# Kernel optimization log

Hardware: AMD Instinct MI355X
Metric: run time of the kernel (lower is better)

The kernel has to match this reference:

```python
import jax, jax.numpy as jnp
import numpy as np

B, N, F = 8, 1024, 256
OUT, REL = 256, 16
NADJ = 7  # ((2 relations + consecutive) * 2 for backward) + self link


def setup_inputs() -> dict:
    key = jax.random.key(0)
    k0, k1, k2, k3, k4 = jax.random.split(key, 5)
    features = jax.random.normal(k0, (B, N, F), dtype=jnp.float32)
    A1 = jax.random.uniform(k1, (B, N, N), dtype=jnp.float32)
    A2 = jax.random.uniform(k2, (B, N, N), dtype=jnp.float32)
    # learned params: one (F+REL, OUT) weight per adjacency matrix, edge embeddings init 'ones', bias (N, OUT)
    W = jax.random.normal(k3, (NADJ, F + REL, OUT), dtype=jnp.float32) * 0.05
    W_edges = jnp.ones((NADJ, REL), dtype=jnp.float32)
    b = jax.random.uniform(k4, (N, OUT), dtype=jnp.float32, minval=-0.05, maxval=0.05)
    return {"features": features, "A1": A1, "A2": A2, "W": W, "W_edges": W_edges, "b": b}


def reference(features, A1, A2, W, W_edges, b):
    # eye = A[0] * zeros(N) + eye(N)  -> batch-broadcast identity [B,N,N]
    eye = jnp.zeros_like(A1) + jnp.eye(N, dtype=A1.dtype)
    # original rolls along axis 0 (batch) of the broadcast identity (faithful replication)
    shifted = jnp.roll(eye, 1, axis=0)
    A_fwd = [A1, A2, shifted]                      # relations + consecutive link
    A_list = A_fwd + [jnp.swapaxes(a, 1, 2) for a in A_fwd]  # backward links
    A_list.append(eye)                             # self links
    A = jnp.stack(A_list, axis=0)                  # [R,B,N,N]

    # concat(features, tile(W_edges[r])) @ W[r] == features @ W[r][:F] + W_edges[r] @ W[r][F:]
    HW = jnp.einsum('bnf,rfo->rbno', features, W[:, :F]) \
         + jnp.einsum('rd,rdo->ro', W_edges, W[:, F:])[:, None, None, :]  # [R,B,N,OUT]
    AHW = jnp.einsum('rbnm,rbmo->rbno', A, HW)     # batched adjacency matmul
    out = jnp.max(AHW, axis=0) + b                 # max-aggregate over relations, add bias
    return out                                     # activation = linear
```

## Files before the change

### kernel.cpp

```cpp
#include <hip/hip_runtime.h>
#include <hip/hip_bf16.h>

#define B_ 8
#define N_ 1024
#define F_ 256
#define OUT_ 256
#define REL_ 16
#define NADJ_ 7

typedef __attribute__((ext_vector_type(8))) _Float16 f16x8;
typedef __attribute__((ext_vector_type(4))) _Float16 f16x4;
typedef __attribute__((ext_vector_type(4))) float f32x4;

__device__ __forceinline__ void gll16(const _Float16* g, _Float16* l) {
    __builtin_amdgcn_global_load_lds(
        (const __attribute__((address_space(1))) void*)g,
        (__attribute__((address_space(3))) void*)l, 16, 0, 0);
}

__device__ __forceinline__ f16x8 cvt8(float4 a, float4 b) {
    return f16x8{(_Float16)a.x, (_Float16)a.y, (_Float16)a.z, (_Float16)a.w,
                 (_Float16)b.x, (_Float16)b.y, (_Float16)b.z, (_Float16)b.w};
}

#define MEMPIN() asm volatile("" ::: "memory")

__constant__ const int c_perm[7] = {0, 1, 3, 4, 2, 5, 6};

__global__ __launch_bounds__(256) void prep_kernel(const float* __restrict__ W,
                                                   const float* __restrict__ We,
                                                   const float* __restrict__ feat,
                                                   float* __restrict__ cb,
                                                   _Float16* __restrict__ WTp,
                                                   _Float16* __restrict__ Fe) {
    int bid = blockIdx.x, tid = threadIdx.x;
    if (bid < 7) {
        int idx = bid * 256 + tid;
        int j = idx / OUT_, o = idx % OUT_;
        int r = c_perm[j];
        const float* Wr = W + (size_t)r * (F_ + REL_) * OUT_;
        float s = 0.f;
#pragma unroll
        for (int d = 0; d < REL_; ++d) s += We[r * REL_ + d] * Wr[(F_ + d) * OUT_ + o];
        cb[idx] = s;
    } else if (bid < 1799) {
        int idx = (bid - 7) * 256 + tid;
        int j = idx >> 16, rem = idx & 65535, o = rem >> 8, f = rem & 255;
        int r = c_perm[j];
        WTp[idx] = (_Float16)W[((size_t)r * (F_ + REL_) + f) * OUT_ + o];
    } else {
        int i = (bid - 1799) * 256 + tid;
        size_t base = (size_t)i * 8;
        float4 a = *(const float4*)(feat + base);
        float4 b = *(const float4*)(feat + base + 4);
        *(f16x8*)(Fe + base) = cvt8(a, b);
    }
}

__global__ __launch_bounds__(256) void hw7_kernel(const _Float16* __restrict__ Fe,
                                                  const _Float16* __restrict__ WTp,
                                                  const float* __restrict__ cb,
                                                  _Float16* __restrict__ HWT,
                                                  _Float16* __restrict__ HWN) {
    __shared__ _Float16 S[3 * 8192];
    const int bid = blockIdx.x, tid = threadIdx.x;
    const int z = bid / 128, rem = bid % 128, bx = rem & 63, by = rem >> 6;
    const bool tr = (z < 4);
    const _Float16* A  = tr ? (WTp + (size_t)z * 65536) : Fe;
    const _Float16* Bt = tr ? Fe : (WTp + (size_t)z * 65536);
    const int m0 = (tr ? by : bx) * 128;
    const int n0 = (tr ? bx : by) * 128;
    const int wave = tid >> 6, lane = tid & 63, lm = lane & 15, q = lane >> 4;
    const int wr = (wave >> 1) * 64, wc = (wave & 1) * 64;
    const int srow = tid >> 2, sk = (tid & 3) * 8;
    const _Float16* ga0 = A + (size_t)(m0 + srow) * F_ + sk;
    const _Float16* ga1 = ga0 + (size_t)64 * F_;
    const _Float16* gb0 = Bt + (size_t)(n0 + srow) * F_ + sk;
    const _Float16* gb1 = gb0 + (size_t)64 * F_;

    f32x4 acc[4][4] = {};
    const int NT = 8;

    {
        gll16(ga0, S + tid * 8);
        gll16(ga1, S + 2048 + tid * 8);
        gll16(gb0, S + 4096 + tid * 8);
        gll16(gb1, S + 6144 + tid * 8);
        MEMPIN();
        gll16(ga0 + 32, S + 8192 + tid * 8);
        gll16(ga1 + 32, S + 8192 + 2048 + tid * 8);
        gll16(gb0 + 32, S + 8192 + 4096 + tid * 8);
        gll16(gb1 + 32, S + 8192 + 6144 + tid * 8);
        asm volatile("s_waitcnt vmcnt(4)" ::: "memory");
        __builtin_amdgcn_s_barrier();
    }
    int cs = 0, ns = 1, fs = 2;
    for (int t = 0; t < NT; ++t) {
        if (t + 2 < NT) {
            const int k = (t + 2) * 32;
            _Float16* sb = S + fs * 8192;
            gll16(ga0 + k, sb + tid * 8);
            gll16(ga1 + k, sb + 2048 + tid * 8);
            gll16(gb0 + k, sb + 4096 + tid * 8);
            gll16(gb1 + k, sb + 6144 + tid * 8);
        }
        {
            const _Float16* Au = S + cs * 8192;
            const _Float16* Bu = Au + 4096;
            f16x8 af[4], bf[4];
#pragma unroll
            for (int i = 0; i < 4; ++i) af[i] = *(const f16x8*)(Au + (wr + i * 16 + lm) * 32 + q * 8);
#pragma unroll
            for (int j = 0; j < 4; ++j) bf[j] = *(const f16x8*)(Bu + (wc + j * 16 + lm) * 32 + q * 8);
            __builtin_amdgcn_s_setprio(1);
#pragma unroll
            for (int i = 0; i < 4; ++i)
#pragma unroll
                for (int j = 0; j < 4; ++j)
                    acc[i][j] = __builtin_amdgcn_mfma_f32_16x16x32_f16(af[i], bf[j], acc[i][j], 0, 0, 0);
            __builtin_amdgcn_s_setprio(0);
        }
        if (t + 1 < NT) {
            if (t + 2 < NT) asm volatile("s_waitcnt vmcnt(4)" ::: "memory");
            else            asm volatile("s_waitcnt vmcnt(0)" ::: "memory");
            __builtin_amdgcn_s_barrier();
        }
        int tmp = cs; cs = ns; ns = fs; fs = tmp;
    }
    const float* cbz = cb + (size_t)z * 256;
    if (tr) {
        _Float16* C = HWT + (size_t)z * ((size_t)256 * 8192);
#pragma unroll
        for (int i = 0; i < 4; ++i)
#pragma unroll
            for (int j = 0; j < 4; ++j)
#pragma unroll
                for (int g = 0; g < 4; ++g) {
                    int row = wr + i * 16 + q * 4 + g;
                    int col = wc + j * 16 + lm;
                    float v = acc[i][j][g] + cbz[m0 + row];
                    C[(size_t)(m0 + row) * 8192 + (n0 + col)] = (_Float16)v;
                }
    } else {
        _Float16* C = HWN + (size_t)(z - 4) * ((size_t)8192 * 256);
#pragma unroll
        for (int i = 0; i < 4; ++i)
#pragma unroll
            for (int j = 0; j < 4; ++j)
#pragma unroll
                for (int g = 0; g < 4; ++g) {
                    int row = wr + i * 16 + q * 4 + g;
                    int col = wc + j * 16 + lm;
                    float v = acc[i][j][g] + cbz[n0 + col];
                    C[(size_t)(m0 + row) * 256 + (n0 + col)] = (_Float16)v;
                }
    }
}

__global__ __launch_bounds__(256) void p2_kernel(const float* __restrict__ A1,
                                                 const float* __restrict__ A2,
                                                 const _Float16* __restrict__ HWT,
                                                 _Float16* __restrict__ AHW) {
    __shared__ _Float16 As[3 * 4096];
    __shared__ _Float16 Bs[3 * 4096];
    const int d = blockIdx.x;
    const int xcd = d & 7, slot = d >> 3;
    const int zz = xcd + 8 * (slot >> 4);
    const int member = (slot >> 3) & 1;
    const int mt = slot & 7;
    const int rr = zz >> 3, b = zz & 7;

    const size_t slab = (size_t)B_ * N_ * OUT_;
    const _Float16* Bt = HWT + (size_t)rr * (256 * 8192) + (size_t)b * 1024;
    _Float16* C = AHW + (size_t)rr * slab + (size_t)b * (N_ * OUT_);
    const int m0 = mt * 128, n0 = member * 128;
    const int tid = threadIdx.x;
    const int wave = tid >> 6, lane = tid & 63, lm = lane & 15, q = lane >> 4;
    const int wr = (wave >> 1) * 64, wc = (wave & 1) * 64;
    const int srow = tid >> 2, sk = (tid & 3) * 8;
    const _Float16* gb0 = Bt + (size_t)(n0 + srow) * 8192 + sk;
    const _Float16* gb1 = gb0 + (size_t)64 * 8192;

    const float* Ag = ((rr & 1) ? A2 : A1) + (size_t)b * N_ * N_;
    f32x4 acc[4][4] = {};
    const int NT = 32;

    auto mfma_step = [&](int st) {
        const _Float16* Au = As + st * 4096;
        const _Float16* Bu = Bs + st * 4096;
        f16x8 af[4], bf[4];
#pragma unroll
        for (int i = 0; i < 4; ++i)
            af[i] = *(const f16x8*)(Au + (wr + i * 16 + lm) * 32 + ((q ^ i) * 8));
#pragma unroll
        for (int j = 0; j < 4; ++j)
            bf[j] = *(const f16x8*)(Bu + (wc + j * 16 + lm) * 32 + q * 8);
        __builtin_amdgcn_s_setprio(1);
#pragma unroll
        for (int i = 0; i < 4; ++i)
#pragma unroll
            for (int j = 0; j < 4; ++j)
                acc[i][j] = __builtin_amdgcn_mfma_f32_16x16x32_f16(af[i], bf[j], acc[i][j], 0, 0, 0);
        __builtin_amdgcn_s_setprio(0);
    };

    if (rr < 2) {
        const float* Ag0 = Ag + (size_t)(m0 + srow) * N_ + sk;
        const float* Ag1 = Ag0 + (size_t)64 * N_;
        const int sx = ((tid & 3) ^ ((tid >> 6) & 3)) * 8;
        float4 p0, p1, p2, p3;
        {
            float4 q0 = *(const float4*)(Ag0);
            float4 q1 = *(const float4*)(Ag0 + 4);
            float4 q2 = *(const float4*)(Ag1);
            float4 q3 = *(const float4*)(Ag1 + 4);
            *(f16x8*)(As + srow * 32 + sx) = cvt8(q0, q1);
            *(f16x8*)(As + 2048 + srow * 32 + sx) = cvt8(q2, q3);
            MEMPIN();
            gll16(gb0, Bs + tid * 8);
            gll16(gb1, Bs + 2048 + tid * 8);
            MEMPIN();
            p0 = *(const float4*)(Ag0 + 32);
            p1 = *(const float4*)(Ag0 + 36);
            p2 = *(const float4*)(Ag1 + 32);
            p3 = *(const float4*)(Ag1 + 36);
            MEMPIN();
            gll16(gb0 + 32, Bs + 4096 + tid * 8);
            gll16(gb1 + 32, Bs + 4096 + 2048 + tid * 8);
            asm volatile("s_waitcnt vmcnt(6)" ::: "memory");
            asm volatile("s_waitcnt lgkmcnt(0)" ::: "memory");
            __builtin_amdgcn_s_barrier();
        }
        int cs = 0, ns = 1, fs = 2;
        for (int t = 0; t < NT; ++t) {
            if (t + 1 < NT) {
                _Float16* la = As + ns * 4096 + srow * 32 + sx;
                *(f16x8*)(la) = cvt8(p0, p1);
                *(f16x8*)(la + 2048) = cvt8(p2, p3);
            }
            MEMPIN();
            if (t + 2 < NT) {
                const int k2 = (t + 2) * 32;
                p0 = *(const float4*)(Ag0 + k2);
                p1 = *(const float4*)(Ag0 + k2 + 4);
                p2 = *(const float4*)(Ag1 + k2);
                p3 = *(const float4*)(Ag1 + k2 + 4);
                MEMPIN();
                gll16(gb0 + k2, Bs + fs * 4096 + tid * 8);
                gll16(gb1 + k2, Bs + fs * 4096 + 2048 + tid * 8);
            }
            mfma_step(cs);
            if (t + 1 < NT) {
                if (t + 2 < NT) asm volatile("s_waitcnt vmcnt(6)" ::: "memory");
                else            asm volatile("s_waitcnt vmcnt(0)" ::: "memory");
                asm volatile("s_waitcnt lgkmcnt(0)" ::: "memory");
                __builtin_amdgcn_s_barrier();
            }
            int tmp = cs; cs = ns; ns = fs; fs = tmp;
        }
    } else {
        const int kk4 = (tid >> 5) * 4;
        const int ms4 = (tid & 31) * 4;
        const int tsw = ((ms4 >> 4) & 3) << 3;
        const int wof = ms4 * 32 + (kk4 ^ tsw);
        const float* gA0 = Ag + (size_t)kk4 * N_ + m0 + ms4;
        float4 r0, r1, r2, r3;
        {
            float4 q0 = *(const float4*)(gA0);
            float4 q1 = *(const float4*)(gA0 + N_);
            float4 q2 = *(const float4*)(gA0 + 2 * N_);
            float4 q3 = *(const float4*)(gA0 + 3 * N_);
            _Float16* wp = As + wof;
            *(f16x4*)(wp + 0 * 32) = f16x4{(_Float16)q0.x, (_Float16)q1.x, (_Float16)q2.x, (_Float16)q3.x};
            *(f16x4*)(wp + 1 * 32) = f16x4{(_Float16)q0.y, (_Float16)q1.y, (_Float16)q2.y, (_Float16)q3.y};
            *(f16x4*)(wp + 2 * 32) = f16x4{(_Float16)q0.z, (_Float16)q1.z, (_Float16)q2.z, (_Float16)q3.z};
            *(f16x4*)(wp + 3 * 32) = f16x4{(_Float16)q0.w, (_Float16)q1.w, (_Float16)q2.w, (_Float16)q3.w};
            MEMPIN();
            gll16(gb0, Bs + tid * 8);
            gll16(gb1, Bs + 2048 + tid * 8);
            MEMPIN();
            const float* p = gA0 + (size_t)32 * N_;
            r0 = *(const float4*)(p);
            r1 = *(const float4*)(p + N_);
            r2 = *(const float4*)(p + 2 * N_);
            r3 = *(const float4*)(p + 3 * N_);
            MEMPIN();
            gll16(gb0 + 32, Bs + 4096 + tid * 8);
            gll16(gb1 + 32, Bs + 4096 + 2048 + tid * 8);
            asm volatile("s_waitcnt vmcnt(6)" ::: "memory");
            asm volatile("s_waitcnt lgkmcnt(0)" ::: "memory");
            __builtin_amdgcn_s_barrier();
        }
        const float* gp = gA0 + (size_t)64 * N_;
        int cs = 0, ns = 1, fs = 2;
        for (int t = 0; t < NT; ++t) {
            if (t + 1 < NT) {
                _Float16* wp = As + ns * 4096 + wof;
                *(f16x4*)(wp + 0 * 32) = f16x4{(_Float16)r0.x, (_Float16)r1.x, (_Float16)r2.x, (_Float16)r3.x};
                *(f16x4*)(wp + 1 * 32) = f16x4{(_Float16)r0.y, (_Float16)r1.y, (_Float16)r2.y, (_Float16)r3.y};
                *(f16x4*)(wp + 2 * 32) = f16x4{(_Float16)r0.z, (_Float16)r1.z, (_Float16)r2.z, (_Float16)r3.z};
                *(f16x4*)(wp + 3 * 32) = f16x4{(_Float16)r0.w, (_Float16)r1.w, (_Float16)r2.w, (_Float16)r3.w};
            }
            MEMPIN();
            if (t + 2 < NT) {
                r0 = *(const float4*)(gp);
                r1 = *(const float4*)(gp + N_);
                r2 = *(const float4*)(gp + 2 * N_);
                r3 = *(const float4*)(gp + 3 * N_);
                gp += (size_t)32 * N_;
                MEMPIN();
                const int k2 = (t + 2) * 32;
                gll16(gb0 + k2, Bs + fs * 4096 + tid * 8);
                gll16(gb1 + k2, Bs + fs * 4096 + 2048 + tid * 8);
            }
            mfma_step(cs);
            if (t + 1 < NT) {
                if (t + 2 < NT) asm volatile("s_waitcnt vmcnt(6)" ::: "memory");
                else            asm volatile("s_waitcnt vmcnt(0)" ::: "memory");
                asm volatile("s_waitcnt lgkmcnt(0)" ::: "memory");
                __builtin_amdgcn_s_barrier();
            }
            int tmp = cs; cs = ns; ns = fs; fs = tmp;
        }
    }
#pragma unroll
    for (int i = 0; i < 4; ++i)
#pragma unroll
        for (int j = 0; j < 4; ++j)
#pragma unroll
            for (int g = 0; g < 4; ++g) {
                int row = wr + i * 16 + q * 4 + g;
                int col = wc + j * 16 + lm;
                C[(size_t)(m0 + row) * 256 + (n0 + col)] = (_Float16)acc[i][j][g];
            }
}

__global__ __launch_bounds__(256) void max_kernel(const _Float16* __restrict__ AHW,
                                                  const _Float16* __restrict__ HWN,
                                                  const float* __restrict__ bias,
                                                  float* __restrict__ out) {
    size_t i = ((size_t)blockIdx.x * 256 + threadIdx.x) * 8;
    const size_t slab = (size_t)B_ * N_ * OUT_;
    float m[8];
    f16x8 v = *(const f16x8*)(AHW + i);
#pragma unroll
    for (int e = 0; e < 8; ++e) m[e] = (float)v[e];
#pragma unroll
    for (int rr = 1; rr < 4; ++rr) {
        f16x8 w = *(const f16x8*)(AHW + rr * slab + i);
#pragma unroll
        for (int e = 0; e < 8; ++e) m[e] = fmaxf(m[e], (float)w[e]);
    }
#pragma unroll
    for (int j = 0; j < 3; ++j) {
        f16x8 w = *(const f16x8*)(HWN + j * slab + i);
#pragma unroll
        for (int e = 0; e < 8; ++e) m[e] = fmaxf(m[e], (float)w[e]);
    }
    size_t bidx = i & ((size_t)N_ * OUT_ - 1);
    float4 b0 = *(const float4*)(bias + bidx);
    float4 b1 = *(const float4*)(bias + bidx + 4);
    float4 o0 = {m[0] + b0.x, m[1] + b0.y, m[2] + b0.z, m[3] + b0.w};
    float4 o1 = {m[4] + b1.x, m[5] + b1.y, m[6] + b1.z, m[7] + b1.w};
    *(float4*)(out + i) = o0;
    *(float4*)(out + i + 4) = o1;
}

__global__ void cbias_kernel(const float* __restrict__ W, const float* __restrict__ We,
                             float* __restrict__ c) {
    int idx = blockIdx.x * 256 + threadIdx.x;
    if (idx >= NADJ_ * OUT_) return;
    int r = idx / OUT_, o = idx % OUT_;
    const float* Wr = W + (size_t)r * (F_ + REL_) * OUT_;
    float s = 0.f;
#pragma unroll
    for (int d = 0; d < REL_; ++d) s += We[r * REL_ + d] * Wr[(F_ + d) * OUT_ + o];
    c[idx] = s;
}

__global__ __launch_bounds__(256) void hw_kernel(const float* __restrict__ feat,
                                                 const float* __restrict__ W,
                                                 const float* __restrict__ cb,
                                                 _Float16* __restrict__ HWb) {
    __shared__ _Float16 As[64][32];
    __shared__ _Float16 Bs[64][32];
    const int mt = blockIdx.x, ct = blockIdx.y;
    const int tid = threadIdx.x, wave = tid >> 6, lane = tid & 63;
    const int r = (ct * 64) / OUT_;
    const int o0 = (ct * 64) % OUT_;
    const float* Bg = W + (size_t)r * (F_ + REL_) * OUT_ + o0;
    const int m0 = mt * 64;
    const int lm = lane & 15, q = lane >> 4;
    f32x4 acc[4] = {};
    for (int k0 = 0; k0 < F_; k0 += 32) {
        {
            int seg = (tid & 3) * 8, m = tid >> 2;
            const float* src = feat + (size_t)(m0 + m) * F_ + k0 + seg;
#pragma unroll
            for (int j = 0; j < 8; ++j) As[m][seg + j] = (_Float16)src[j];
        }
        {
            int kk = tid >> 3, ns = (tid & 7) * 8;
            const float* src = Bg + (size_t)(k0 + kk) * OUT_ + ns;
#pragma unroll
            for (int j = 0; j < 8; ++j) Bs[ns + j][kk] = (_Float16)src[j];
        }
        __syncthreads();
        f16x8 a = *(const f16x8*)&As[wave * 16 + lm][q * 8];
#pragma unroll
        for (int c4 = 0; c4 < 4; ++c4) {
            f16x8 b = *(const f16x8*)&Bs[c4 * 16 + lm][q * 8];
            acc[c4] = __builtin_amdgcn_mfma_f32_16x16x32_f16(a, b, acc[c4], 0, 0, 0);
        }
        __syncthreads();
    }
#pragma unroll
    for (int c4 = 0; c4 < 4; ++c4)
#pragma unroll
        for (int g = 0; g < 4; ++g) {
            int row = wave * 16 + (lane >> 4) * 4 + g;
            int col = c4 * 16 + lm;
            float v = acc[c4][g] + cb[r * OUT_ + o0 + col];
            HWb[((size_t)r * B_ * N_ + m0 + row) * OUT_ + o0 + col] = (_Float16)v;
        }
}

__global__ __launch_bounds__(256) void agg_kernel(const float* __restrict__ A1,
                                                  const float* __restrict__ A2,
                                                  const _Float16* __restrict__ HWb,
                                                  const float* __restrict__ bias,
                                                  float* __restrict__ out) {
    __shared__ _Float16 As[64][32];
    __shared__ _Float16 Bs[64][32];
    const int b = blockIdx.z, nt = blockIdx.y, ot = blockIdx.x;
    const int tid = threadIdx.x, wave = tid >> 6, lane = tid & 63;
    const int n0 = nt * 64, o0 = ot * 64;
    const int lm = lane & 15, q = lane >> 4;
    const size_t rstride = (size_t)B_ * N_ * OUT_;
    f32x4 mx[4];
#pragma unroll
    for (int i = 0; i < 4; ++i) mx[i] = f32x4{-1e30f, -1e30f, -1e30f, -1e30f};
#pragma unroll 1
    for (int rr = 0; rr < 4; ++rr) {
        const float* Ag = ((rr & 1) ? A2 : A1) + (size_t)b * N_ * N_;
        const bool tr = (rr >= 2);
        const int r = (rr < 2) ? rr : rr + 1;
        const _Float16* Bg = HWb + (size_t)r * rstride + (size_t)b * N_ * OUT_ + o0;
        f32x4 acc[4] = {};
        for (int k0 = 0; k0 < N_; k0 += 32) {
            if (!tr) {
                int seg = (tid & 3) * 8, m = tid >> 2;
                const float* src = Ag + (size_t)(n0 + m) * N_ + k0 + seg;
#pragma unroll
                for (int j = 0; j < 8; ++j) As[m][seg + j] = (_Float16)src[j];
            } else {
                int kk = tid >> 3, ms = (tid & 7) * 8;
                const float* src = Ag + (size_t)(k0 + kk) * N_ + n0 + ms;
#pragma unroll
                for (int j = 0; j < 8; ++j) As[ms + j][kk] = (_Float16)src[j];
            }
            {
                int kk = tid >> 3, ns = (tid & 7) * 8;
                const _Float16* src = Bg + (size_t)(k0 + kk) * OUT_ + ns;
#pragma unroll
                for (int j = 0; j < 8; ++j) Bs[ns + j][kk] = src[j];
            }
            __syncthreads();
            f16x8 a = *(const f16x8*)&As[wave * 16 + lm][q * 8];
#pragma unroll
            for (int c4 = 0; c4 < 4; ++c4) {
                f16x8 bb = *(const f16x8*)&Bs[c4 * 16 + lm][q * 8];
                acc[c4] = __builtin_amdgcn_mfma_f32_16x16x32_f16(a, bb, acc[c4], 0, 0, 0);
            }
            __syncthreads();
        }
#pragma unroll
        for (int c4 = 0; c4 < 4; ++c4)
#pragma unroll
            for (int g = 0; g < 4; ++g) mx[c4][g] = fmaxf(mx[c4][g], acc[c4][g]);
    }
#pragma unroll
    for (int c4 = 0; c4 < 4; ++c4)
#pragma unroll
        for (int g = 0; g < 4; ++g) {
            int row = wave * 16 + (lane >> 4) * 4 + g;
            int col = c4 * 16 + lm;
            size_t pos = ((size_t)b * N_ + n0 + row) * OUT_ + o0 + col;
            float v = mx[c4][g];
            v = fmaxf(v, (float)HWb[2 * rstride + pos]);
            v = fmaxf(v, (float)HWb[5 * rstride + pos]);
            v = fmaxf(v, (float)HWb[6 * rstride + pos]);
            out[pos] = v + bias[((size_t)(n0 + row)) * OUT_ + o0 + col];
        }
}

extern "C" void kernel_launch(void* const* d_in, const int* in_sizes, int n_in,
                              void* d_out, int out_size, void* d_ws, size_t ws_size,
                              hipStream_t stream) {
    const float* feat = (const float*)d_in[0];
    const float* A1   = (const float*)d_in[1];
    const float* A2   = (const float*)d_in[2];
    const float* W    = (const float*)d_in[3];
    const float* We   = (const float*)d_in[4];
    const float* bias = (const float*)d_in[5];
    float* out = (float*)d_out;

    const size_t OFF_CB   = 0;
    const size_t OFF_WT   = 8192;
    const size_t OFF_FE   = 1048576;
    const size_t OFF_HWT  = 5242880;
    const size_t OFF_HWN  = 22020096;
    const size_t OFF_AHW  = 34603008;
    const size_t WS_NEEDED = 51380224;

    if (ws_size >= WS_NEEDED) {
        float*    cbp = (float*)((char*)d_ws + OFF_CB);
        _Float16* WTp = (_Float16*)((char*)d_ws + OFF_WT);
        _Float16* Fe  = (_Float16*)((char*)d_ws + OFF_FE);
        _Float16* HWT = (_Float16*)((char*)d_ws + OFF_HWT);
        _Float16* HWN = (_Float16*)((char*)d_ws + OFF_HWN);
        _Float16* AHW = (_Float16*)((char*)d_ws + OFF_AHW);

        prep_kernel<<<2823, 256, 0, stream>>>(W, We, feat, cbp, WTp, Fe);
        hw7_kernel<<<896, 256, 0, stream>>>(Fe, WTp, cbp, HWT, HWN);
        p2_kernel<<<512, 256, 0, stream>>>(A1, A2, HWT, AHW);
        max_kernel<<<1024, 256, 0, stream>>>(AHW, HWN, bias, out);
    } else {
        float* cb = (float*)d_ws;
        _Float16* HWb = (_Float16*)((char*)d_ws + 8192);
        cbias_kernel<<<7, 256, 0, stream>>>(W, We, cb);
        hw_kernel<<<dim3(128, 28), 256, 0, stream>>>(feat, W, cb, HWb);
        agg_kernel<<<dim3(4, 16, 8), 256, 0, stream>>>(A1, A2, HWb, bias, out);
    }
}
```

Baseline: 174.4 us.

## Split-K the adjacency GEMM into two halves, loading operands directly to registers

The aggregation GEMM kernel now splits the K dimension in two, doubling the grid to 1024 blocks and writing two partial AHW slabs that the max kernel sums before taking the max. The non-transposed path drops LDS staging entirely and loads A (fp32, converted in registers) and B fragments straight from global memory with register double buffering. The transposed path uses a 64-wide K tile with a new swizzle and reads B directly from global. This targets low occupancy and tail effects with only 512 blocks, at the cost of extra partial-sum traffic, a larger workspace and possibly uncoalesced direct global fragment loads.

Result: slower. 200.7 us (+15.1%).

```diff
diff --git a/kernel.cpp b/kernel.cpp
--- a/kernel.cpp
+++ b/kernel.cpp
@@ -161,166 +161,139 @@
                                                  const float* __restrict__ A2,
                                                  const _Float16* __restrict__ HWT,
                                                  _Float16* __restrict__ AHW) {
-    __shared__ _Float16 As[3 * 4096];
-    __shared__ _Float16 Bs[3 * 4096];
+    __shared__ _Float16 As[2 * 8192];
     const int d = blockIdx.x;
     const int xcd = d & 7, slot = d >> 3;
-    const int zz = xcd + 8 * (slot >> 4);
+    const int mt = slot & 7;
     const int member = (slot >> 3) & 1;
-    const int mt = slot & 7;
-    const int rr = zz >> 3, b = zz & 7;
+    const int kh = (slot >> 4) & 1;
+    const int rr = slot >> 5;
+    const int b = xcd;
 
     const size_t slab = (size_t)B_ * N_ * OUT_;
     const _Float16* Bt = HWT + (size_t)rr * (256 * 8192) + (size_t)b * 1024;
-    _Float16* C = AHW + (size_t)rr * slab + (size_t)b * (N_ * OUT_);
-    const int m0 = mt * 128, n0 = member * 128;
+    _Float16* C = AHW + (size_t)kh * (4 * slab) + (size_t)rr * slab + (size_t)b * (N_ * OUT_);
+    const int m0 = mt * 128, n0 = member * 128, kbase = kh * 512;
     const int tid = threadIdx.x;
     const int wave = tid >> 6, lane = tid & 63, lm = lane & 15, q = lane >> 4;
     const int wr = (wave >> 1) * 64, wc = (wave & 1) * 64;
-    const int srow = tid >> 2, sk = (tid & 3) * 8;
-    const _Float16* gb0 = Bt + (size_t)(n0 + srow) * 8192 + sk;
-    const _Float16* gb1 = gb0 + (size_t)64 * 8192;
 
     const float* Ag = ((rr & 1) ? A2 : A1) + (size_t)b * N_ * N_;
     f32x4 acc[4][4] = {};
-    const int NT = 32;
-
-    auto mfma_step = [&](int st) {
-        const _Float16* Au = As + st * 4096;
-        const _Float16* Bu = Bs + st * 4096;
-        f16x8 af[4], bf[4];
+
+    const _Float16* brow[4];
+#pragma unroll
+    for (int j = 0; j < 4; ++j)
+        brow[j] = Bt + (size_t)(n0 + wc + j * 16 + lm) * 8192 + kbase + q * 8;
+
+    if (rr < 2) {
+        const float* arow[4];
 #pragma unroll
         for (int i = 0; i < 4; ++i)
-            af[i] = *(const f16x8*)(Au + (wr + i * 16 + lm) * 32 + ((q ^ i) * 8));
-#pragma unroll
-        for (int j = 0; j < 4; ++j)
-            bf[j] = *(const f16x8*)(Bu + (wc + j * 16 + lm) * 32 + q * 8);
-        __builtin_amdgcn_s_setprio(1);
-#pragma unroll
-        for (int i = 0; i < 4; ++i)
-#pragma unroll
-            for (int j = 0; j < 4; ++j)
-                acc[i][j] = __builtin_amdgcn_mfma_f32_16x16x32_f16(af[i], bf[j], acc[i][j], 0, 0, 0);
-        __builtin_amdgcn_s_setprio(0);
-    };
-
-    if (rr < 2) {
-        const float* Ag0 = Ag + (size_t)(m0 + srow) * N_ + sk;
-        const float* Ag1 = Ag0 + (size_t)64 * N_;
-        const int sx = ((tid & 3) ^ ((tid >> 6) & 3)) * 8;
-        float4 p0, p1, p2, p3;
-        {
-            float4 q0 = *(const float4*)(Ag0);
-            float4 q1 = *(const float4*)(Ag0 + 4);
-            float4 q2 = *(const float4*)(Ag1);
-            float4 q3 = *(const float4*)(Ag1 + 4);
-            *(f16x8*)(As + srow * 32 + sx) = cvt8(q0, q1);
-            *(f16x8*)(As + 2048 + srow * 32 + sx) = cvt8(q2, q3);
-            MEMPIN();
-            gll16(gb0, Bs + tid * 8);
-            gll16(gb1, Bs + 2048 + tid * 8);
-            MEMPIN();
-            p0 = *(const float4*)(Ag0 + 32);
-            p1 = *(const float4*)(Ag0 + 36);
-            p2 = *(const float4*)(Ag1 + 32);
-            p3 = *(const float4*)(Ag1 + 36);
-            MEMPIN();
-            gll16(gb0 + 32, Bs + 4096 + tid * 8);
-            gll16(gb1 + 32, Bs + 4096 + 2048 + tid * 8);
-            asm volatile("s_waitcnt vmcnt(6)" ::: "memory");
+            arow[i] = Ag + (size_t)(m0 + wr + i * 16 + lm) * N_ + kbase + q * 8;
+
+        float4 a0[4][2];
+        f16x8 b0[4];
+#pragma unroll
+        for (int i = 0; i < 4; ++i) {
+            a0[i][0] = *(const float4*)(arow[i]);
+            a0[i][1] = *(const float4*)(arow[i] + 4);
+        }
+#pragma unroll
+        for (int j = 0; j < 4; ++j) b0[j] = *(const f16x8*)(brow[j]);
+#pragma unroll
+        for (int t = 0; t < 16; ++t) {
+            float4 a1[4][2];
+            f16x8 b1[4];
+            if (t < 15) {
+#pragma unroll
+                for (int i = 0; i < 4; ++i) {
+                    a1[i][0] = *(const float4*)(arow[i] + (t + 1) * 32);
+                    a1[i][1] = *(const float4*)(arow[i] + (t + 1) * 32 + 4);
+                }
+#pragma unroll
+                for (int j = 0; j < 4; ++j) b1[j] = *(const f16x8*)(brow[j] + (t + 1) * 32);
+            }
+            f16x8 af[4];
+#pragma unroll
+            for (int i = 0; i < 4; ++i) af[i] = cvt8(a0[i][0], a0[i][1]);
+            __builtin_amdgcn_s_setprio(1);
+#pragma unroll
+            for (int i = 0; i < 4; ++i)
+#pragma unroll
+                for (int j = 0; j < 4; ++j)
+                    acc[i][j] = __builtin_amdgcn_mfma_f32_16x16x32_f16(af[i], b0[j], acc[i][j], 0, 0, 0);
+            __builtin_amdgcn_s_setprio(0);
+            if (t < 15) {
+#pragma unroll
+                for (int i = 0; i < 4; ++i) { a0[i][0] = a1[i][0]; a0[i][1] = a1[i][1]; }
+#pragma unroll
+                for (int j = 0; j < 4; ++j) b0[j] = b1[j];
+            }
+        }
+    } else {
+        const int lk = (tid >> 4) * 4, mc8 = (tid & 15) * 8;
+        const int shi = (tid & 15) >> 1;
+        const float* gA = Ag + (size_t)(kbase + lk) * N_ + m0 + mc8;
+        f32x4 rlo[4], rhi[4];
+
+        auto RD = [&](int t) {
+            const float* p = gA + (size_t)t * 64 * N_;
+#pragma unroll
+            for (int k = 0; k < 4; ++k) {
+                rlo[k] = *(const f32x4*)(p + (size_t)k * N_);
+                rhi[k] = *(const f32x4*)(p + (size_t)k * N_ + 4);
+            }
+        };
+        auto WRS = [&](int st) {
+            _Float16* base = As + st * 8192;
+            const int g0 = lk >> 3, kof = lk & 7;
+#pragma unroll
+            for (int c = 0; c < 4; ++c) {
+                int r = mc8 + c, s = c ^ shi;
+                *(f16x4*)(base + r * 64 + ((g0 ^ s) << 3) + kof) =
+                    f16x4{(_Float16)rlo[0][c], (_Float16)rlo[1][c], (_Float16)rlo[2][c], (_Float16)rlo[3][c]};
+            }
+#pragma unroll
+            for (int c = 0; c < 4; ++c) {
+                int r = mc8 + 4 + c, s = (4 + c) ^ shi;
+                *(f16x4*)(base + r * 64 + ((g0 ^ s) << 3) + kof) =
+                    f16x4{(_Float16)rhi[0][c], (_Float16)rhi[1][c], (_Float16)rhi[2][c], (_Float16)rhi[3][c]};
+            }
+        };
+
+        RD(0);
+        WRS(0);
+        RD(1);
+        asm volatile("s_waitcnt lgkmcnt(0)" ::: "memory");
+        __builtin_amdgcn_s_barrier();
+
+#pragma unroll
+        for (int t = 0; t < 8; ++t) {
+            const int cs = t & 1, ns = cs ^ 1;
+            if (t < 7) WRS(ns);
+            if (t < 6) RD(t + 2);
+#pragma unroll
+            for (int h = 0; h < 2; ++h) {
+                f16x8 af[4], bf[4];
+#pragma unroll
+                for (int i = 0; i < 4; ++i) {
+                    int r = wr + i * 16 + lm;
+                    int s = (lm & 7) ^ (((wr >> 4) + i) & 7);
+                    af[i] = *(const f16x8*)(As + cs * 8192 + r * 64 + (((h * 4 + q) ^ s) << 3));
+                }
+#pragma unroll
+                for (int j = 0; j < 4; ++j) bf[j] = *(const f16x8*)(brow[j] + t * 64 + h * 32);
+                __builtin_amdgcn_s_setprio(1);
+#pragma unroll
+                for (int i = 0; i < 4; ++i)
+#pragma unroll
+                    for (int j = 0; j < 4; ++j)
+                        acc[i][j] = __builtin_amdgcn_mfma_f32_16x16x32_f16(af[i], bf[j], acc[i][j], 0, 0, 0);
+                __builtin_amdgcn_s_setprio(0);
+            }
             asm volatile("s_waitcnt lgkmcnt(0)" ::: "memory");
             __builtin_amdgcn_s_barrier();
-        }
-        int cs = 0, ns = 1, fs = 2;
-        for (int t = 0; t < NT; ++t) {
-            if (t + 1 < NT) {
-                _Float16* la = As + ns * 4096 + srow * 32 + sx;
-                *(f16x8*)(la) = cvt8(p0, p1);
-                *(f16x8*)(la + 2048) = cvt8(p2, p3);
-            }
-            MEMPIN();
-            if (t + 2 < NT) {
-                const int k2 = (t + 2) * 32;
-                p0 = *(const float4*)(Ag0 + k2);
-                p1 = *(const float4*)(Ag0 + k2 + 4);
-                p2 = *(const float4*)(Ag1 + k2);
-                p3 = *(const float4*)(Ag1 + k2 + 4);
-                MEMPIN();
-                gll16(gb0 + k2, Bs + fs * 4096 + tid * 8);
-                gll16(gb1 + k2, Bs + fs * 4096 + 2048 + tid * 8);
-            }
-            mfma_step(cs);
-            if (t + 1 < NT) {
-                if (t + 2 < NT) asm volatile("s_waitcnt vmcnt(6)" ::: "memory");
-                else            asm volatile("s_waitcnt vmcnt(0)" ::: "memory");
-                asm volatile("s_waitcnt lgkmcnt(0)" ::: "memory");
-                __builtin_amdgcn_s_barrier();
-            }
-            int tmp = cs; cs = ns; ns = fs; fs = tmp;
-        }
-    } else {
-        const int kk4 = (tid >> 5) * 4;
-        const int ms4 = (tid & 31) * 4;
-        const int tsw = ((ms4 >> 4) & 3) << 3;
-        const int wof = ms4 * 32 + (kk4 ^ tsw);
-        const float* gA0 = Ag + (size_t)kk4 * N_ + m0 + ms4;
-        float4 r0, r1, r2, r3;
-        {
-            float4 q0 = *(const float4*)(gA0);
-            float4 q1 = *(const float4*)(gA0 + N_);
-            float4 q2 = *(const float4*)(gA0 + 2 * N_);
-            float4 q3 = *(const float4*)(gA0 + 3 * N_);
-            _Float16* wp = As + wof;
-            *(f16x4*)(wp + 0 * 32) = f16x4{(_Float16)q0.x, (_Float16)q1.x, (_Float16)q2.x, (_Float16)q3.x};
-            *(f16x4*)(wp + 1 * 32) = f16x4{(_Float16)q0.y, (_Float16)q1.y, (_Float16)q2.y, (_Float16)q3.y};
-            *(f16x4*)(wp + 2 * 32) = f16x4{(_Float16)q0.z, (_Float16)q1.z, (_Float16)q2.z, (_Float16)q3.z};
-            *(f16x4*)(wp + 3 * 32) = f16x4{(_Float16)q0.w, (_Float16)q1.w, (_Float16)q2.w, (_Float16)q3.w};
-            MEMPIN();
-            gll16(gb0, Bs + tid * 8);
-            gll16(gb1, Bs + 2048 + tid * 8);
-            MEMPIN();
-            const float* p = gA0 + (size_t)32 * N_;
-            r0 = *(const float4*)(p);
-            r1 = *(const float4*)(p + N_);
-            r2 = *(const float4*)(p + 2 * N_);
-            r3 = *(const float4*)(p + 3 * N_);
-            MEMPIN();
-            gll16(gb0 + 32, Bs + 4096 + tid * 8);
-            gll16(gb1 + 32, Bs + 4096 + 2048 + tid * 8);
-            asm volatile("s_waitcnt vmcnt(6)" ::: "memory");
-            asm volatile("s_waitcnt lgkmcnt(0)" ::: "memory");
-            __builtin_amdgcn_s_barrier();
-        }
-        const float* gp = gA0 + (size_t)64 * N_;
-        int cs = 0, ns = 1, fs = 2;
-        for (int t = 0; t < NT; ++t) {
-            if (t + 1 < NT) {
-                _Float16* wp = As + ns * 4096 + wof;
-                *(f16x4*)(wp + 0 * 32) = f16x4{(_Float16)r0.x, (_Float16)r1.x, (_Float16)r2.x, (_Float16)r3.x};
-                *(f16x4*)(wp + 1 * 32) = f16x4{(_Float16)r0.y, (_Float16)r1.y, (_Float16)r2.y, (_Float16)r3.y};
-                *(f16x4*)(wp + 2 * 32) = f16x4{(_Float16)r0.z, (_Float16)r1.z, (_Float16)r2.z, (_Float16)r3.z};
-                *(f16x4*)(wp + 3 * 32) = f16x4{(_Float16)r0.w, (_Float16)r1.w, (_Float16)r2.w, (_Float16)r3.w};
-            }
-            MEMPIN();
-            if (t + 2 < NT) {
-                r0 = *(const float4*)(gp);
-                r1 = *(const float4*)(gp + N_);
-                r2 = *(const float4*)(gp + 2 * N_);
-                r3 = *(const float4*)(gp + 3 * N_);
-                gp += (size_t)32 * N_;
-                MEMPIN();
-                const int k2 = (t + 2) * 32;
-                gll16(gb0 + k2, Bs + fs * 4096 + tid * 8);
-                gll16(gb1 + k2, Bs + fs * 4096 + 2048 + tid * 8);
-            }
-            mfma_step(cs);
-            if (t + 1 < NT) {
-                if (t + 2 < NT) asm volatile("s_waitcnt vmcnt(6)" ::: "memory");
-                else            asm volatile("s_waitcnt vmcnt(0)" ::: "memory");
-                asm volatile("s_waitcnt lgkmcnt(0)" ::: "memory");
-                __builtin_amdgcn_s_barrier();
-            }
-            int tmp = cs; cs = ns; ns = fs; fs = tmp;
         }
     }
 #pragma unroll
@@ -341,15 +314,20 @@
                                                   float* __restrict__ out) {
     size_t i = ((size_t)blockIdx.x * 256 + threadIdx.x) * 8;
     const size_t slab = (size_t)B_ * N_ * OUT_;
+    const size_t HS = 4 * slab;
     float m[8];
-    f16x8 v = *(const f16x8*)(AHW + i);
-#pragma unroll
-    for (int e = 0; e < 8; ++e) m[e] = (float)v[e];
+    {
+        f16x8 v0 = *(const f16x8*)(AHW + i);
+        f16x8 v1 = *(const f16x8*)(AHW + HS + i);
+#pragma unroll
+        for (int e = 0; e < 8; ++e) m[e] = (float)v0[e] + (float)v1[e];
+    }
 #pragma unroll
     for (int rr = 1; rr < 4; ++rr) {
-        f16x8 w = *(const f16x8*)(AHW + rr * slab + i);
-#pragma unroll
-        for (int e = 0; e < 8; ++e) m[e] = fmaxf(m[e], (float)w[e]);
+        f16x8 v0 = *(const f16x8*)(AHW + rr * slab + i);
+        f16x8 v1 = *(const f16x8*)(AHW + HS + rr * slab + i);
+#pragma unroll
+        for (int e = 0; e < 8; ++e) m[e] = fmaxf(m[e], (float)v0[e] + (float)v1[e]);
     }
 #pragma unroll
     for (int j = 0; j < 3; ++j) {
@@ -511,7 +489,7 @@
     const size_t OFF_HWT  = 5242880;
     const size_t OFF_HWN  = 22020096;
     const size_t OFF_AHW  = 34603008;
-    const size_t WS_NEEDED = 51380224;
+    const size_t WS_NEEDED = 68157440;
 
     if (ws_size >= WS_NEEDED) {
         float*    cbp = (float*)((char*)d_ws + OFF_CB);
@@ -523,7 +501,7 @@
 
         prep_kernel<<<2823, 256, 0, stream>>>(W, We, feat, cbp, WTp, Fe);
         hw7_kernel<<<896, 256, 0, stream>>>(Fe, WTp, cbp, HWT, HWN);
-        p2_kernel<<<512, 256, 0, stream>>>(A1, A2, HWT, AHW);
+        p2_kernel<<<1024, 256, 0, stream>>>(A1, A2, HWT, AHW);
         max_kernel<<<1024, 256, 0, stream>>>(AHW, HWN, bias, out);
     } else {
         float* cb = (float*)d_ws;
```

## Pre-convert adjacency to fp16 and split aggregation GEMM along K

Applied to the files above, without the earlier changes.

Adds extra blocks to the HW GEMM kernel that convert A1/A2 from fp32 to fp16 into a new workspace buffer, relayouts HWT per batch, and splits the p2 aggregation GEMM into two K halves with twice the blocks. The non-transposed path now uses direct global-to-LDS loads instead of register conversion. The max kernel sums the two partial results before the max. This aims to raise parallelism and simplify loads, but it adds a full fp16 copy of the adjacency (extra write and read traffic) and doubles the partial-result traffic.

Result: no change. 173.5 us (-0.6%).

```diff
diff --git a/kernel.cpp b/kernel.cpp
--- a/kernel.cpp
+++ b/kernel.cpp
@@ -57,13 +57,24 @@
     }
 }
 
-__global__ __launch_bounds__(256) void hw7_kernel(const _Float16* __restrict__ Fe,
+__global__ __launch_bounds__(256) void hw7_kernel(const float* __restrict__ A1,
+                                                  const float* __restrict__ A2,
+                                                  const _Float16* __restrict__ Fe,
                                                   const _Float16* __restrict__ WTp,
                                                   const float* __restrict__ cb,
                                                   _Float16* __restrict__ HWT,
-                                                  _Float16* __restrict__ HWN) {
+                                                  _Float16* __restrict__ HWN,
+                                                  _Float16* __restrict__ Af) {
     __shared__ _Float16 S[3 * 8192];
     const int bid = blockIdx.x, tid = threadIdx.x;
+    if (bid >= 896) {
+        size_t idx = ((size_t)(bid - 896) * 256 + tid) * 8;
+        const float* src = (idx < 8388608) ? (A1 + idx) : (A2 + (idx - 8388608));
+        float4 a = *(const float4*)(src);
+        float4 b = *(const float4*)(src + 4);
+        *(f16x8*)(Af + idx) = cvt8(a, b);
+        return;
+    }
     const int z = bid / 128, rem = bid % 128, bx = rem & 63, by = rem >> 6;
     const bool tr = (z < 4);
     const _Float16* A  = tr ? (WTp + (size_t)z * 65536) : Fe;
@@ -129,7 +140,8 @@
     }
     const float* cbz = cb + (size_t)z * 256;
     if (tr) {
-        _Float16* C = HWT + (size_t)z * ((size_t)256 * 8192);
+        _Float16* C = HWT + (size_t)z * (8 * 256 * 1024) + (size_t)(n0 >> 10) * (256 * 1024);
+        const int nl = n0 & 1023;
 #pragma unroll
         for (int i = 0; i < 4; ++i)
 #pragma unroll
@@ -139,7 +151,7 @@
                     int row = wr + i * 16 + q * 4 + g;
                     int col = wc + j * 16 + lm;
                     float v = acc[i][j][g] + cbz[m0 + row];
-                    C[(size_t)(m0 + row) * 8192 + (n0 + col)] = (_Float16)v;
+                    C[(size_t)(m0 + row) * 1024 + nl + col] = (_Float16)v;
                 }
     } else {
         _Float16* C = HWN + (size_t)(z - 4) * ((size_t)8192 * 256);
@@ -157,73 +169,99 @@
     }
 }
 
-__global__ __launch_bounds__(256) void p2_kernel(const float* __restrict__ A1,
-                                                 const float* __restrict__ A2,
+__global__ __launch_bounds__(256) void p2_kernel(const _Float16* __restrict__ Af,
                                                  const _Float16* __restrict__ HWT,
                                                  _Float16* __restrict__ AHW) {
     __shared__ _Float16 As[3 * 4096];
     __shared__ _Float16 Bs[3 * 4096];
     const int d = blockIdx.x;
-    const int xcd = d & 7, slot = d >> 3;
-    const int zz = xcd + 8 * (slot >> 4);
+    const int b = d & 7, slot = d >> 3;
+    const int kh = slot >> 6;
+    const int rr = (slot >> 4) & 3;
     const int member = (slot >> 3) & 1;
     const int mt = slot & 7;
-    const int rr = zz >> 3, b = zz & 7;
 
     const size_t slab = (size_t)B_ * N_ * OUT_;
-    const _Float16* Bt = HWT + (size_t)rr * (256 * 8192) + (size_t)b * 1024;
-    _Float16* C = AHW + (size_t)rr * slab + (size_t)b * (N_ * OUT_);
-    const int m0 = mt * 128, n0 = member * 128;
+    const _Float16* Ag = Af + (size_t)((rr & 1) * 8 + b) * 1048576;
+    const _Float16* Bt = HWT + (size_t)(rr * 8 + b) * (256 * 1024);
+    _Float16* C = AHW + (size_t)kh * (4 * slab) + (size_t)rr * slab + (size_t)b * (N_ * OUT_);
+    const int m0 = mt * 128, n0 = member * 128, kbase = kh * 512;
     const int tid = threadIdx.x;
     const int wave = tid >> 6, lane = tid & 63, lm = lane & 15, q = lane >> 4;
     const int wr = (wave >> 1) * 64, wc = (wave & 1) * 64;
     const int srow = tid >> 2, sk = (tid & 3) * 8;
-    const _Float16* gb0 = Bt + (size_t)(n0 + srow) * 8192 + sk;
-    const _Float16* gb1 = gb0 + (size_t)64 * 8192;
-
-    const float* Ag = ((rr & 1) ? A2 : A1) + (size_t)b * N_ * N_;
+    const _Float16* gb0 = Bt + (size_t)(n0 + srow) * 1024 + kbase + sk;
+    const _Float16* gb1 = gb0 + (size_t)64 * 1024;
+
     f32x4 acc[4][4] = {};
-    const int NT = 32;
-
-    auto mfma_step = [&](int st) {
-        const _Float16* Au = As + st * 4096;
-        const _Float16* Bu = Bs + st * 4096;
-        f16x8 af[4], bf[4];
-#pragma unroll
-        for (int i = 0; i < 4; ++i)
-            af[i] = *(const f16x8*)(Au + (wr + i * 16 + lm) * 32 + ((q ^ i) * 8));
-#pragma unroll
-        for (int j = 0; j < 4; ++j)
-            bf[j] = *(const f16x8*)(Bu + (wc + j * 16 + lm) * 32 + q * 8);
-        __builtin_amdgcn_s_setprio(1);
-#pragma unroll
-        for (int i = 0; i < 4; ++i)
-#pragma unroll
-            for (int j = 0; j < 4; ++j)
-                acc[i][j] = __builtin_amdgcn_mfma_f32_16x16x32_f16(af[i], bf[j], acc[i][j], 0, 0, 0);
-        __builtin_amdgcn_s_setprio(0);
-    };
+    const int NT = 16;
 
     if (rr < 2) {
-        const float* Ag0 = Ag + (size_t)(m0 + srow) * N_ + sk;
-        const float* Ag1 = Ag0 + (size_t)64 * N_;
-        const int sx = ((tid & 3) ^ ((tid >> 6) & 3)) * 8;
-        float4 p0, p1, p2, p3;
+        const _Float16* ga0 = Ag + (size_t)(m0 + srow) * 1024 + kbase + sk;
+        const _Float16* ga1 = ga0 + (size_t)64 * 1024;
+        auto ST = [&](int st, int k) {
+            gll16(ga0 + k, As + st * 4096 + tid * 8);
+            gll16(ga1 + k, As + st * 4096 + 2048 + tid * 8);
+            gll16(gb0 + k, Bs + st * 4096 + tid * 8);
+            gll16(gb1 + k, Bs + st * 4096 + 2048 + tid * 8);
+        };
+        ST(0, 0);
+        MEMPIN();
+        ST(1, 32);
+        asm volatile("s_waitcnt vmcnt(4)" ::: "memory");
+        __builtin_amdgcn_s_barrier();
+        int cs = 0, ns = 1, fs = 2;
+        for (int t = 0; t < NT; ++t) {
+            if (t + 2 < NT) ST(fs, (t + 2) * 32);
+            {
+                const _Float16* Au = As + cs * 4096;
+                const _Float16* Bu = Bs + cs * 4096;
+                f16x8 af[4], bf[4];
+#pragma unroll
+                for (int i = 0; i < 4; ++i) af[i] = *(const f16x8*)(Au + (wr + i * 16 + lm) * 32 + q * 8);
+#pragma unroll
+                for (int j = 0; j < 4; ++j) bf[j] = *(const f16x8*)(Bu + (wc + j * 16 + lm) * 32 + q * 8);
+                __builtin_amdgcn_s_setprio(1);
+#pragma unroll
+                for (int i = 0; i < 4; ++i)
+#pragma unroll
+                    for (int j = 0; j < 4; ++j)
+                        acc[i][j] = __builtin_amdgcn_mfma_f32_16x16x32_f16(af[i], bf[j], acc[i][j], 0, 0, 0);
+                __builtin_amdgcn_s_setprio(0);
+            }
+            if (t + 1 < NT) {
+                if (t + 2 < NT) asm volatile("s_waitcnt vmcnt(4)" ::: "memory");
+                else            asm volatile("s_waitcnt vmcnt(0)" ::: "memory");
+                __builtin_amdgcn_s_barrier();
+            }
+            int tmp = cs; cs = ns; ns = fs; fs = tmp;
+        }
+    } else {
+        const int kk4 = (tid >> 5) * 4;
+        const int ms4 = (tid & 31) * 4;
+        const int tsw = ((ms4 >> 4) & 3) << 3;
+        const int wof = ms4 * 32 + (kk4 ^ tsw);
+        const _Float16* gA0 = Ag + (size_t)(kbase + kk4) * 1024 + m0 + ms4;
+        f16x4 r0, r1, r2, r3;
         {
-            float4 q0 = *(const float4*)(Ag0);
-            float4 q1 = *(const float4*)(Ag0 + 4);
-            float4 q2 = *(const float4*)(Ag1);
-            float4 q3 = *(const float4*)(Ag1 + 4);
-            *(f16x8*)(As + srow * 32 + sx) = cvt8(q0, q1);
-            *(f16x8*)(As + 2048 + srow * 32 + sx) = cvt8(q2, q3);
+            f16x4 q0 = *(const f16x4*)(gA0);
+            f16x4 q1 = *(const f16x4*)(gA0 + 1024);
+            f16x4 q2 = *(const f16x4*)(gA0 + 2048);
+            f16x4 q3 = *(const f16x4*)(gA0 + 3072);
+            _Float16* wp = As + wof;
+            *(f16x4*)(wp + 0 * 32) = f16x4{q0[0], q1[0], q2[0], q3[0]};
+            *(f16x4*)(wp + 1 * 32) = f16x4{q0[1], q1[1], q2[1], q3[1]};
+            *(f16x4*)(wp + 2 * 32) = f16x4{q0[2], q1[2], q2[2], q3[2]};
+            *(f16x4*)(wp + 3 * 32) = f16x4{q0[3], q1[3], q2[3], q3[3]};
             MEMPIN();
             gll16(gb0, Bs + tid * 8);
             gll16(gb1, Bs + 2048 + tid * 8);
             MEMPIN();
-            p0 = *(const float4*)(Ag0 + 32);
-            p1 = *(const float4*)(Ag0 + 36);
-            p2 = *(const float4*)(Ag1 + 32);
-            p3 = *(const float4*)(Ag1 + 36);
+            const _Float16* p = gA0 + (size_t)32 * 1024;
+            r0 = *(const f16x4*)(p);
+            r1 = *(const f16x4*)(p + 1024);
+            r2 = *(const f16x4*)(p + 2048);
+            r3 = *(const f16x4*)(p + 3072);
             MEMPIN();
             gll16(gb0 + 32, Bs + 4096 + tid * 8);
             gll16(gb1 + 32, Bs + 4096 + 2048 + tid * 8);
@@ -231,89 +269,46 @@
             asm volatile("s_waitcnt lgkmcnt(0)" ::: "memory");
             __builtin_amdgcn_s_barrier();
         }
-        int cs = 0, ns = 1, fs = 2;
-        for (int t = 0; t < NT; ++t) {
-            if (t + 1 < NT) {
-                _Float16* la = As + ns * 4096 + srow * 32 + sx;
-                *(f16x8*)(la) = cvt8(p0, p1);
-                *(f16x8*)(la + 2048) = cvt8(p2, p3);
-            }
-            MEMPIN();
-            if (t + 2 < NT) {
-                const int k2 = (t + 2) * 32;
-                p0 = *(const float4*)(Ag0 + k2);
-                p1 = *(const float4*)(Ag0 + k2 + 4);
-                p2 = *(const float4*)(Ag1 + k2);
-                p3 = *(const float4*)(Ag1 + k2 + 4);
-                MEMPIN();
-                gll16(gb0 + k2, Bs + fs * 4096 + tid * 8);
-                gll16(gb1 + k2, Bs + fs * 4096 + 2048 + tid * 8);
-            }
-            mfma_step(cs);
-            if (t + 1 < NT) {
-                if (t + 2 < NT) asm volatile("s_waitcnt vmcnt(6)" ::: "memory");
-                else            asm volatile("s_waitcnt vmcnt(0)" ::: "memory");
-                asm volatile("s_waitcnt lgkmcnt(0)" ::: "memory");
-                __builtin_amdgcn_s_barrier();
-            }
-            int tmp = cs; cs = ns; ns = fs; fs = tmp;
-        }
-    } else {
-        const int kk4 = (tid >> 5) * 4;
-        const int ms4 = (tid & 31) * 4;
-        const int tsw = ((ms4 >> 4) & 3) << 3;
-        const int wof = ms4 * 32 + (kk4 ^ tsw);
-        const float* gA0 = Ag + (size_t)kk4 * N_ + m0 + ms4;
-        float4 r0, r1, r2, r3;
-        {
-            float4 q0 = *(const float4*)(gA0);
-            float4 q1 = *(const float4*)(gA0 + N_);
-            float4 q2 = *(const float4*)(gA0 + 2 * N_);
-            float4 q3 = *(const float4*)(gA0 + 3 * N_);
-            _Float16* wp = As + wof;
-            *(f16x4*)(wp + 0 * 32) = f16x4{(_Float16)q0.x, (_Float16)q1.x, (_Float16)q2.x, (_Float16)q3.x};
-            *(f16x4*)(wp + 1 * 32) = f16x4{(_Float16)q0.y, (_Float16)q1.y, (_Float16)q2.y, (_Float16)q3.y};
-            *(f16x4*)(wp + 2 * 32) = f16x4{(_Float16)q0.z, (_Float16)q1.z, (_Float16)q2.z, (_Float16)q3.z};
-            *(f16x4*)(wp + 3 * 32) = f16x4{(_Float16)q0.w, (_Float16)q1.w, (_Float16)q2.w, (_Float16)q3.w};
-            MEMPIN();
-            gll16(gb0, Bs + tid * 8);
-            gll16(gb1, Bs + 2048 + tid * 8);
-            MEMPIN();
-            const float* p = gA0 + (size_t)32 * N_;
-            r0 = *(const float4*)(p);
-            r1 = *(const float4*)(p + N_);
-            r2 = *(const float4*)(p + 2 * N_);
-            r3 = *(const float4*)(p + 3 * N_);
-            MEMPIN();
-            gll16(gb0 + 32, Bs + 4096 + tid * 8);
-            gll16(gb1 + 32, Bs + 4096 + 2048 + tid * 8);
-            asm volatile("s_waitcnt vmcnt(6)" ::: "memory");
-            asm volatile("s_waitcnt lgkmcnt(0)" ::: "memory");
-            __builtin_amdgcn_s_barrier();
-        }
-        const float* gp = gA0 + (size_t)64 * N_;
+        const _Float16* gp = gA0 + (size_t)64 * 1024;
         int cs = 0, ns = 1, fs = 2;
         for (int t = 0; t < NT; ++t) {
             if (t + 1 < NT) {
                 _Float16* wp = As + ns * 4096 + wof;
-                *(f16x4*)(wp + 0 * 32) = f16x4{(_Float16)r0.x, (_Float16)r1.x, (_Float16)r2.x, (_Float16)r3.x};
-                *(f16x4*)(wp + 1 * 32) = f16x4{(_Float16)r0.y, (_Float16)r1.y, (_Float16)r2.y, (_Float16)r3.y};
-                *(f16x4*)(wp + 2 * 32) = f16x4{(_Float16)r0.z, (_Float16)r1.z, (_Float16)r2.z, (_Float16)r3.z};
-                *(f16x4*)(wp + 3 * 32) = f16x4{(_Float16)r0.w, (_Float16)r1.w, (_Float16)r2.w, (_Float16)r3.w};
+                *(f16x4*)(wp + 0 * 32) = f16x4{r0[0], r1[0], r2[0], r3[0]};
+                *(f16x4*)(wp + 1 * 32) = f16x4{r0[1], r1[1], r2[1], r3[1]};
+                *(f16x4*)(wp + 2 * 32) = f16x4{r0[2], r1[2], r2[2], r3[2]};
+                *(f16x4*)(wp + 3 * 32) = f16x4{r0[3], r1[3], r2[3], r3[3]};
             }
             MEMPIN();
             if (t + 2 < NT) {
-                r0 = *(const float4*)(gp);
-                r1 = *(const float4*)(gp + N_);
-                r2 = *(const float4*)(gp + 2 * N_);
-                r3 = *(const float4*)(gp + 3 * N_);
-                gp += (size_t)32 * N_;
+                r0 = *(const f16x4*)(gp);
+                r1 = *(const f16x4*)(gp + 1024);
+                r2 = *(const f16x4*)(gp + 2048);
+                r3 = *(const f16x4*)(gp + 3072);
+                gp += (size_t)32 * 1024;
                 MEMPIN();
                 const int k2 = (t + 2) * 32;
                 gll16(gb0 + k2, Bs + fs * 4096 + tid * 8);
                 gll16(gb1 + k2, Bs + fs * 4096 + 2048 + tid * 8);
             }
-            mfma_step(cs);
+            {
+                const _Float16* Au = As + cs * 4096;
+                const _Float16* Bu = Bs + cs * 4096;
+                f16x8 af[4], bf[4];
+#pragma unroll
+                for (int i = 0; i < 4; ++i)
+                    af[i] = *(const f16x8*)(Au + (wr + i * 16 + lm) * 32 + ((q ^ i) * 8));
+#pragma unroll
+                for (int j = 0; j < 4; ++j)
+                    bf[j] = *(const f16x8*)(Bu + (wc + j * 16 + lm) * 32 + q * 8);
+                __builtin_amdgcn_s_setprio(1);
+#pragma unroll
+                for (int i = 0; i < 4; ++i)
+#pragma unroll
+                    for (int j = 0; j < 4; ++j)
+                        acc[i][j] = __builtin_amdgcn_mfma_f32_16x16x32_f16(af[i], bf[j], acc[i][j], 0, 0, 0);
+                __builtin_amdgcn_s_setprio(0);
+            }
             if (t + 1 < NT) {
                 if (t + 2 < NT) asm volatile("s_waitcnt vmcnt(6)" ::: "memory");
                 else            asm volatile("s_waitcnt vmcnt(0)" ::: "memory");
@@ -341,15 +336,20 @@
                                                   float* __restrict__ out) {
     size_t i = ((size_t)blockIdx.x * 256 + threadIdx.x) * 8;
     const size_t slab = (size_t)B_ * N_ * OUT_;
+    const size_t HS = 4 * slab;
     float m[8];
-    f16x8 v = *(const f16x8*)(AHW + i);
-#pragma unroll
-    for (int e = 0; e < 8; ++e) m[e] = (float)v[e];
+    {
+        f16x8 v0 = *(const f16x8*)(AHW + i);
+        f16x8 v1 = *(const f16x8*)(AHW + HS + i);
+#pragma unroll
+        for (int e = 0; e < 8; ++e) m[e] = (float)v0[e] + (float)v1[e];
+    }
 #pragma unroll
     for (int rr = 1; rr < 4; ++rr) {
-        f16x8 w = *(const f16x8*)(AHW + rr * slab + i);
-#pragma unroll
-        for (int e = 0; e < 8; ++e) m[e] = fmaxf(m[e], (float)w[e]);
+        f16x8 v0 = *(const f16x8*)(AHW + rr * slab + i);
+        f16x8 v1 = *(const f16x8*)(AHW + HS + rr * slab + i);
+#pragma unroll
+        for (int e = 0; e < 8; ++e) m[e] = fmaxf(m[e], (float)v0[e] + (float)v1[e]);
     }
 #pragma unroll
     for (int j = 0; j < 3; ++j) {
@@ -511,7 +511,8 @@
     const size_t OFF_HWT  = 5242880;
     const size_t OFF_HWN  = 22020096;
     const size_t OFF_AHW  = 34603008;
-    const size_t WS_NEEDED = 51380224;
+    const size_t OFF_AF   = 68157440;
+    const size_t WS_NEEDED = 101711872;
 
     if (ws_size >= WS_NEEDED) {
         float*    cbp = (float*)((char*)d_ws + OFF_CB);
@@ -520,10 +521,11 @@
         _Float16* HWT = (_Float16*)((char*)d_ws + OFF_HWT);
         _Float16* HWN = (_Float16*)((char*)d_ws + OFF_HWN);
         _Float16* AHW = (_Float16*)((char*)d_ws + OFF_AHW);
+        _Float16* Afp = (_Float16*)((char*)d_ws + OFF_AF);
 
         prep_kernel<<<2823, 256, 0, stream>>>(W, We, feat, cbp, WTp, Fe);
-        hw7_kernel<<<896, 256, 0, stream>>>(Fe, WTp, cbp, HWT, HWN);
-        p2_kernel<<<512, 256, 0, stream>>>(A1, A2, HWT, AHW);
+        hw7_kernel<<<9088, 256, 0, stream>>>(A1, A2, Fe, WTp, cbp, HWT, HWN, Afp);
+        p2_kernel<<<1024, 256, 0, stream>>>(Afp, HWT, AHW);
         max_kernel<<<1024, 256, 0, stream>>>(AHW, HWN, bias, out);
     } else {
         float* cb = (float*)d_ws;
```
